# Kernel tuning notes

Hardware: AMD Instinct MI355X
Metric: run time of the kernel (lower is better)

Reference implementation:

```python
import jax, jax.numpy as jnp
import numpy as np

NEG_INF = -9e15  # same masking constant as the original
LEAKY_ALPHA = 0.2  # tf.nn.leaky_relu default


def setup_inputs() -> dict:
    key = jax.random.key(0)
    k1, k2, k3, k4 = jax.random.split(key, 4)
    N, D, F = 8192, 256, 64
    features = jax.random.normal(k1, (N, D), dtype=jnp.float32)
    adj = jax.random.randint(k2, (N, N), 0, 2, dtype=jnp.int32)
    W = jax.random.normal(k3, (D, F), dtype=jnp.float32) * (1.0 / np.sqrt(D))
    a = jax.random.normal(k4, (2 * F, 1), dtype=jnp.float32) * 0.1
    return {"features": features, "adj": adj, "W": W, "a": a}


def reference(features, adj, W, a):
    # h = X W : [N, F]
    h = features @ W
    F = h.shape[1]
    # a^T [h_i || h_j] = (h a1)_i + (h a2)_j  -- avoids the N*N*2F concat tensor
    a1, a2 = a[:F], a[F:]            # [F,1] each
    e = jax.nn.leaky_relu((h @ a1) + (h @ a2).T, LEAKY_ALPHA)  # [N, N]
    scores = jnp.where(adj > 0, e, jnp.float32(NEG_INF))
    attention = jax.nn.softmax(scores, axis=1)                  # masked softmax over neighbors j
    h_prime = attention @ h                                     # [N, F]
    return jax.nn.elu(h_prime)
```

## Files before the change

kernel.cpp:

```cpp
#include <hip/hip_runtime.h>
#include <hip/hip_bf16.h>
#include <math.h>

#define NN 8192
#define DD 256
#define FF 64
#define NSPLIT 16
#define JCHUNK (NN / NSPLIT)

typedef __attribute__((ext_vector_type(8))) short bf16x8;
typedef __attribute__((ext_vector_type(4))) float f32x4;

__device__ __forceinline__ float lrelu(float x) { return fmaxf(x, 0.2f * x); }
__device__ __forceinline__ short f2bf(float x) {
  union { __hip_bfloat16 b; short s; } u;
  u.b = __float2bfloat16(x);
  return u.s;
}

__global__ __launch_bounds__(256) void k_pre(const float* __restrict__ W,
                                             ushort* __restrict__ WT) {
  const int e4 = (blockIdx.x * 256 + threadIdx.x) * 4;
  const float4 wv = *(const float4*)(W + e4);
  const int k = e4 >> 6, d = e4 & 63;
  WT[(d + 0) * DD + k] = (ushort)f2bf(wv.x);
  WT[(d + 1) * DD + k] = (ushort)f2bf(wv.y);
  WT[(d + 2) * DD + k] = (ushort)f2bf(wv.z);
  WT[(d + 3) * DD + k] = (ushort)f2bf(wv.w);
}

__global__ __launch_bounds__(256) void k_h(
    const float* __restrict__ feat, const ushort* __restrict__ WT,
    const float* __restrict__ a, ushort* __restrict__ hT,
    float* __restrict__ s1, float* __restrict__ s2) {
  __shared__ float sp1[4][16], sp2[4][16];
  const int t = threadIdx.x, lane = t & 63, w = t >> 6;
  const int il = lane & 15, kg = lane >> 4;
  const int ibase = blockIdx.x * 16;
  const int d = w * 16 + il;
  const float* frow = feat + (size_t)(ibase + il) * DD + kg * 8;
  const ushort* wrow = WT + (size_t)d * DD + kg * 8;
  f32x4 acc = {0.f, 0.f, 0.f, 0.f};
#pragma unroll
  for (int k0 = 0; k0 < DD; k0 += 32) {
    const float4 fa = *(const float4*)(frow + k0);
    const float4 fb = *(const float4*)(frow + k0 + 4);
    bf16x8 av;
    av[0] = f2bf(fa.x); av[1] = f2bf(fa.y); av[2] = f2bf(fa.z); av[3] = f2bf(fa.w);
    av[4] = f2bf(fb.x); av[5] = f2bf(fb.y); av[6] = f2bf(fb.z); av[7] = f2bf(fb.w);
    const bf16x8 bv = *(const bf16x8*)(wrow + k0);
    acc = __builtin_amdgcn_mfma_f32_16x16x32_bf16(av, bv, acc, 0, 0, 0);
  }
  ushort4 hv;
  hv.x = (ushort)f2bf(acc[0]);
  hv.y = (ushort)f2bf(acc[1]);
  hv.z = (ushort)f2bf(acc[2]);
  hv.w = (ushort)f2bf(acc[3]);
  *(ushort4*)(hT + (size_t)d * NN + ibase + kg * 4) = hv;
  const float a1v = a[d], a2v = a[FF + d];
#pragma unroll
  for (int r = 0; r < 4; ++r) {
    float v1 = acc[r] * a1v;
    float v2 = acc[r] * a2v;
#pragma unroll
    for (int m = 1; m <= 8; m <<= 1) {
      v1 += __shfl_xor(v1, m);
      v2 += __shfl_xor(v2, m);
    }
    if (il == 0) {
      sp1[w][kg * 4 + r] = v1;
      sp2[w][kg * 4 + r] = v2;
    }
  }
  __syncthreads();
  if (t < 16) {
    s1[ibase + t] = sp1[0][t] + sp1[1][t] + sp1[2][t] + sp1[3][t];
    s2[ibase + t] = sp2[0][t] + sp2[1][t] + sp2[2][t] + sp2[3][t];
  }
}

__global__ __launch_bounds__(256) void k_attn(
    const int* __restrict__ adj, const ushort* __restrict__ hT,
    const float* __restrict__ s1g, const float* __restrict__ s2g,
    float* __restrict__ pacc, float* __restrict__ pl) {
  __shared__ float tr[4][16][65];
  const int t = threadIdx.x;
  const int lane = t & 63, w = t >> 6;
  const int il = lane & 15, kg = lane >> 4;
  const int ig = blockIdx.x >> 4, js = blockIdx.x & 15;
  const int ibase = ig * 64 + w * 16;
  const int i = ibase + il;
  const float s1v = s1g[i];
  const float mi = lrelu(s1v + 8.0f);
  float lacc = 0.f;
  f32x4 acc[4] = {{0,0,0,0},{0,0,0,0},{0,0,0,0},{0,0,0,0}};
  const size_t arow = (size_t)i * NN;
  const int jbase = js * JCHUNK + kg * 8;
#pragma unroll 4
  for (int jc = 0; jc < JCHUNK / 32; ++jc) {
    const int jl = jbase + jc * 32;
    const int4 av0 = *(const int4*)(adj + arow + jl);
    const int4 av1 = *(const int4*)(adj + arow + jl + 4);
    const float4 sa = *(const float4*)(s2g + jl);
    const float4 sb = *(const float4*)(s2g + jl + 4);
    float p0 = av0.x ? __expf(lrelu(s1v + sa.x) - mi) : 0.f;
    float p1 = av0.y ? __expf(lrelu(s1v + sa.y) - mi) : 0.f;
    float p2 = av0.z ? __expf(lrelu(s1v + sa.z) - mi) : 0.f;
    float p3 = av0.w ? __expf(lrelu(s1v + sa.w) - mi) : 0.f;
    float p4 = av1.x ? __expf(lrelu(s1v + sb.x) - mi) : 0.f;
    float p5 = av1.y ? __expf(lrelu(s1v + sb.y) - mi) : 0.f;
    float p6 = av1.z ? __expf(lrelu(s1v + sb.z) - mi) : 0.f;
    float p7 = av1.w ? __expf(lrelu(s1v + sb.w) - mi) : 0.f;
    lacc += ((p0 + p1) + (p2 + p3)) + ((p4 + p5) + (p6 + p7));
    bf16x8 pb;
    pb[0] = f2bf(p0); pb[1] = f2bf(p1); pb[2] = f2bf(p2); pb[3] = f2bf(p3);
    pb[4] = f2bf(p4); pb[5] = f2bf(p5); pb[6] = f2bf(p6); pb[7] = f2bf(p7);
#pragma unroll
    for (int f = 0; f < 4; ++f) {
      const bf16x8 hv = *(const bf16x8*)(hT + (size_t)(f * 16 + il) * NN + jl);
      acc[f] = __builtin_amdgcn_mfma_f32_16x16x32_bf16(hv, pb, acc[f], 0, 0, 0);
    }
  }
  lacc += __shfl_xor(lacc, 16);
  lacc += __shfl_xor(lacc, 32);
  if (lane < 16) pl[(size_t)js * NN + ibase + lane] = lacc;
#pragma unroll
  for (int f = 0; f < 4; ++f)
#pragma unroll
    for (int r = 0; r < 4; ++r) tr[w][il][f * 16 + kg * 4 + r] = acc[f][r];
#pragma unroll
  for (int r = 0; r < 16; ++r)
    pacc[((size_t)js * NN + ibase + r) * FF + lane] = tr[w][r][lane];
}

__global__ __launch_bounds__(256) void k_combine(
    const float* __restrict__ pacc, const float* __restrict__ pl,
    float* __restrict__ out) {
  const int idx = blockIdx.x * 256 + threadIdx.x;
  const int i = idx >> 6;
  float s = 0.f, L = 0.f;
#pragma unroll
  for (int sp = 0; sp < NSPLIT; ++sp) {
    s += pacc[(size_t)sp * NN * FF + idx];
    L += pl[(size_t)sp * NN + i];
  }
  float x = s / fmaxf(L, 1e-30f);
  out[idx] = x > 0.f ? x : expm1f(x);
}

extern "C" void kernel_launch(void* const* d_in, const int* in_sizes, int n_in,
                              void* d_out, int out_size, void* d_ws, size_t ws_size,
                              hipStream_t stream) {
  const float* feat = (const float*)d_in[0];
  const int* adj = (const int*)d_in[1];
  const float* W = (const float*)d_in[2];
  const float* a = (const float*)d_in[3];
  float* out = (float*)d_out;

  ushort* hT = (ushort*)d_ws;
  ushort* WT = hT + (size_t)FF * NN;
  float* s1 = (float*)(WT + (size_t)FF * DD);
  float* s2 = s1 + NN;
  float* pl = s2 + NN;
  float* pacc = pl + (size_t)NSPLIT * NN;

  hipLaunchKernelGGL(k_pre, dim3(DD * FF / 1024), dim3(256), 0, stream, W, WT);
  hipLaunchKernelGGL(k_h, dim3(NN / 16), dim3(256), 0, stream, feat, WT, a, hT, s1, s2);
  hipLaunchKernelGGL(k_attn, dim3((NN / 64) * NSPLIT), dim3(256), 0, stream,
                     adj, hT, s1, s2, pacc, pl);
  hipLaunchKernelGGL(k_combine, dim3(NN * FF / 256), dim3(256), 0, stream,
                     pacc, pl, out);
}
```

Baseline: 417.3 us.

## Coalesce adjacency loads via LDS staging and fragment-major h layout

```diff
diff --git a/kernel.cpp b/kernel.cpp
--- a/kernel.cpp
+++ b/kernel.cpp
@@ -7,15 +7,22 @@
 #define FF 64
 #define NSPLIT 16
 #define JCHUNK (NN / NSPLIT)
+#define CT 128
+#define NT (JCHUNK / CT)
 
 typedef __attribute__((ext_vector_type(8))) short bf16x8;
 typedef __attribute__((ext_vector_type(4))) float f32x4;
 
 __device__ __forceinline__ float lrelu(float x) { return fmaxf(x, 0.2f * x); }
-__device__ __forceinline__ short f2bf(float x) {
-  union { __hip_bfloat16 b; short s; } u;
+__device__ __forceinline__ ushort f2bf(float x) {
+  union { __hip_bfloat16 b; ushort s; } u;
   u.b = __float2bfloat16(x);
   return u.s;
+}
+__device__ __forceinline__ float bf2f(ushort s) {
+  union { uint u; float f; } v;
+  v.u = (uint)s << 16;
+  return v.f;
 }
 
 __global__ __launch_bounds__(256) void k_pre(const float* __restrict__ W,
@@ -23,15 +30,15 @@
   const int e4 = (blockIdx.x * 256 + threadIdx.x) * 4;
   const float4 wv = *(const float4*)(W + e4);
   const int k = e4 >> 6, d = e4 & 63;
-  WT[(d + 0) * DD + k] = (ushort)f2bf(wv.x);
-  WT[(d + 1) * DD + k] = (ushort)f2bf(wv.y);
-  WT[(d + 2) * DD + k] = (ushort)f2bf(wv.z);
-  WT[(d + 3) * DD + k] = (ushort)f2bf(wv.w);
+  WT[(d + 0) * DD + k] = f2bf(wv.x);
+  WT[(d + 1) * DD + k] = f2bf(wv.y);
+  WT[(d + 2) * DD + k] = f2bf(wv.z);
+  WT[(d + 3) * DD + k] = f2bf(wv.w);
 }
 
 __global__ __launch_bounds__(256) void k_h(
     const float* __restrict__ feat, const ushort* __restrict__ WT,
-    const float* __restrict__ a, ushort* __restrict__ hT,
+    const float* __restrict__ a, ushort* __restrict__ hTf,
     float* __restrict__ s1, float* __restrict__ s2) {
   __shared__ float sp1[4][16], sp2[4][16];
   const int t = threadIdx.x, lane = t & 63, w = t >> 6;
@@ -52,11 +59,16 @@
     acc = __builtin_amdgcn_mfma_f32_16x16x32_bf16(av, bv, acc, 0, 0, 0);
   }
   ushort4 hv;
-  hv.x = (ushort)f2bf(acc[0]);
-  hv.y = (ushort)f2bf(acc[1]);
-  hv.z = (ushort)f2bf(acc[2]);
-  hv.w = (ushort)f2bf(acc[3]);
-  *(ushort4*)(hT + (size_t)d * NN + ibase + kg * 4) = hv;
+  hv.x = f2bf(acc[0]);
+  hv.y = f2bf(acc[1]);
+  hv.z = f2bf(acc[2]);
+  hv.w = f2bf(acc[3]);
+  {
+    const int i0q = ibase + kg * 4;
+    const size_t hb = ((size_t)(w * 256 + (i0q >> 5)) * 64 +
+                       ((i0q >> 3) & 3) * 16 + il) * 8 + (i0q & 7);
+    *(ushort4*)(hTf + hb) = hv;
+  }
   const float a1v = a[d], a2v = a[FF + d];
 #pragma unroll
   for (int r = 0; r < 4; ++r) {
@@ -80,57 +92,72 @@
 }
 
 __global__ __launch_bounds__(256) void k_attn(
-    const int* __restrict__ adj, const ushort* __restrict__ hT,
+    const int* __restrict__ adj, const ushort* __restrict__ hTf,
     const float* __restrict__ s1g, const float* __restrict__ s2g,
     float* __restrict__ pacc, float* __restrict__ pl) {
-  __shared__ float tr[4][16][65];
+  __shared__ __align__(16) char smem[4][4480];
+  __shared__ float s1w[4][16];
   const int t = threadIdx.x;
   const int lane = t & 63, w = t >> 6;
   const int il = lane & 15, kg = lane >> 4;
   const int ig = blockIdx.x >> 4, js = blockIdx.x & 15;
-  const int ibase = ig * 64 + w * 16;
-  const int i = ibase + il;
-  const float s1v = s1g[i];
-  const float mi = lrelu(s1v + 8.0f);
+  const int rbase = ig * 64 + w * 16;
+  const int jwin0 = js * JCHUNK;
+  char* const smemw = smem[w];
+
+  if (lane < 16) s1w[w][lane] = s1g[rbase + lane];
+  const int arow = lane >> 5;
+  const int acol = (lane & 31) * 4;
+  const int* ap = adj + (size_t)(rbase + arow) * NN + jwin0 + acol;
+
   float lacc = 0.f;
   f32x4 acc[4] = {{0,0,0,0},{0,0,0,0},{0,0,0,0},{0,0,0,0}};
-  const size_t arow = (size_t)i * NN;
-  const int jbase = js * JCHUNK + kg * 8;
-#pragma unroll 4
-  for (int jc = 0; jc < JCHUNK / 32; ++jc) {
-    const int jl = jbase + jc * 32;
-    const int4 av0 = *(const int4*)(adj + arow + jl);
-    const int4 av1 = *(const int4*)(adj + arow + jl + 4);
-    const float4 sa = *(const float4*)(s2g + jl);
-    const float4 sb = *(const float4*)(s2g + jl + 4);
-    float p0 = av0.x ? __expf(lrelu(s1v + sa.x) - mi) : 0.f;
-    float p1 = av0.y ? __expf(lrelu(s1v + sa.y) - mi) : 0.f;
-    float p2 = av0.z ? __expf(lrelu(s1v + sa.z) - mi) : 0.f;
-    float p3 = av0.w ? __expf(lrelu(s1v + sa.w) - mi) : 0.f;
-    float p4 = av1.x ? __expf(lrelu(s1v + sb.x) - mi) : 0.f;
-    float p5 = av1.y ? __expf(lrelu(s1v + sb.y) - mi) : 0.f;
-    float p6 = av1.z ? __expf(lrelu(s1v + sb.z) - mi) : 0.f;
-    float p7 = av1.w ? __expf(lrelu(s1v + sb.w) - mi) : 0.f;
-    lacc += ((p0 + p1) + (p2 + p3)) + ((p4 + p5) + (p6 + p7));
-    bf16x8 pb;
-    pb[0] = f2bf(p0); pb[1] = f2bf(p1); pb[2] = f2bf(p2); pb[3] = f2bf(p3);
-    pb[4] = f2bf(p4); pb[5] = f2bf(p5); pb[6] = f2bf(p6); pb[7] = f2bf(p7);
-#pragma unroll
-    for (int f = 0; f < 4; ++f) {
-      const bf16x8 hv = *(const bf16x8*)(hT + (size_t)(f * 16 + il) * NN + jl);
-      acc[f] = __builtin_amdgcn_mfma_f32_16x16x32_bf16(hv, pb, acc[f], 0, 0, 0);
+
+  for (int tile = 0; tile < NT; ++tile) {
+    const int jt = jwin0 + tile * CT;
+    const float4 s2v = *(const float4*)(s2g + jt + acol);
+#pragma unroll
+    for (int rep = 0; rep < 8; ++rep) {
+      const int r = rep * 2 + arow;
+      const int4 av = *(const int4*)(ap + (size_t)rep * 2 * NN + tile * CT);
+      const float s1v = s1w[w][r];
+      const float mi = lrelu(s1v + 8.0f);
+      ushort4 pk;
+      pk.x = av.x ? f2bf(__expf(lrelu(s1v + s2v.x) - mi)) : (ushort)0;
+      pk.y = av.y ? f2bf(__expf(lrelu(s1v + s2v.y) - mi)) : (ushort)0;
+      pk.z = av.z ? f2bf(__expf(lrelu(s1v + s2v.z) - mi)) : (ushort)0;
+      pk.w = av.w ? f2bf(__expf(lrelu(s1v + s2v.w) - mi)) : (ushort)0;
+      const int swz = r * 256 + ((acol * 2) ^ ((r & 7) << 4));
+      *(ushort4*)(smemw + swz) = pk;
+    }
+#pragma unroll
+    for (int sb = 0; sb < 4; ++sb) {
+      const int coff = (sb * 32 + kg * 8) * 2;
+      const bf16x8 pb = *(const bf16x8*)(smemw + il * 256 + (coff ^ ((il & 7) << 4)));
+      float ps = 0.f;
+#pragma unroll
+      for (int e = 0; e < 8; ++e) ps += bf2f((ushort)pb[e]);
+      lacc += ps;
+      const int j32 = (jt >> 5) + sb;
+#pragma unroll
+      for (int f = 0; f < 4; ++f) {
+        const bf16x8 hv =
+            *(const bf16x8*)(hTf + ((size_t)(f * 256 + j32) * 64 + lane) * 8);
+        acc[f] = __builtin_amdgcn_mfma_f32_16x16x32_bf16(hv, pb, acc[f], 0, 0, 0);
+      }
     }
   }
   lacc += __shfl_xor(lacc, 16);
   lacc += __shfl_xor(lacc, 32);
-  if (lane < 16) pl[(size_t)js * NN + ibase + lane] = lacc;
+  if (lane < 16) pl[(size_t)js * NN + rbase + lane] = lacc;
+  float (*tr)[65] = (float(*)[65])smemw;
 #pragma unroll
   for (int f = 0; f < 4; ++f)
 #pragma unroll
-    for (int r = 0; r < 4; ++r) tr[w][il][f * 16 + kg * 4 + r] = acc[f][r];
+    for (int r = 0; r < 4; ++r) tr[il][f * 16 + kg * 4 + r] = acc[f][r];
 #pragma unroll
   for (int r = 0; r < 16; ++r)
-    pacc[((size_t)js * NN + ibase + r) * FF + lane] = tr[w][r][lane];
+    pacc[((size_t)js * NN + rbase + r) * FF + lane] = tr[r][lane];
 }
 
 __global__ __launch_bounds__(256) void k_combine(
@@ -157,17 +184,17 @@
   const float* a = (const float*)d_in[3];
   float* out = (float*)d_out;
 
-  ushort* hT = (ushort*)d_ws;
-  ushort* WT = hT + (size_t)FF * NN;
+  ushort* hTf = (ushort*)d_ws;
+  ushort* WT = hTf + (size_t)FF * NN;
   float* s1 = (float*)(WT + (size_t)FF * DD);
   float* s2 = s1 + NN;
   float* pl = s2 + NN;
   float* pacc = pl + (size_t)NSPLIT * NN;
 
   hipLaunchKernelGGL(k_pre, dim3(DD * FF / 1024), dim3(256), 0, stream, W, WT);
-  hipLaunchKernelGGL(k_h, dim3(NN / 16), dim3(256), 0, stream, feat, WT, a, hT, s1, s2);
+  hipLaunchKernelGGL(k_h, dim3(NN / 16), dim3(256), 0, stream, feat, WT, a, hTf, s1, s2);
   hipLaunchKernelGGL(k_attn, dim3((NN / 64) * NSPLIT), dim3(256), 0, stream,
-                     adj, hT, s1, s2, pacc, pl);
+                     adj, hTf, s1, s2, pacc, pl);
   hipLaunchKernelGGL(k_combine, dim3(NN * FF / 256), dim3(256), 0, stream,
                      pacc, pl, out);
 }
```

Result: faster. 386.9 us (-7.3%).
